# Kernel optimization log

Measured on AMD Instinct MI355X. Metric: run time of the kernel, lower is better.

The kernel has to match this reference:

```python
import jax, jax.numpy as jnp
import numpy as np

N, IN, H, C = 50000, 128, 256, 64
E_G, E_K = 600000, 800000
MLP_H = H // 2  # multiplier=2 (residual=False)
EPS = 1e-5


def _w(k, i, o):
    return (jax.random.normal(k, (i, o), jnp.float32) * np.float32(1.0 / np.sqrt(i)))


def setup_inputs() -> dict:
    key = jax.random.key(0)
    ks = jax.random.split(key, 32)
    inp = {
        "feat": jax.random.normal(ks[0], (N, IN), jnp.float32),
        "g_src": jax.random.randint(ks[1], (E_G,), 0, N, jnp.int32),
        "g_dst": jax.random.randint(ks[2], (E_G,), 0, N, jnp.int32),
        "k_src": jax.random.randint(ks[3], (E_K,), 0, N, jnp.int32),
        "k_dst": jax.random.randint(ks[4], (E_K,), 0, N, jnp.int32),
        # local GraphSAGE: 3 SAGEConv layers (IN->H, H->H, H->H)
        "lw_self_0": _w(ks[5], IN, H), "lw_neigh_0": _w(ks[6], IN, H), "lb_0": jnp.zeros((H,), jnp.float32),
        "lw_self_1": _w(ks[7], H, H),  "lw_neigh_1": _w(ks[8], H, H),  "lb_1": jnp.zeros((H,), jnp.float32),
        "lw_self_2": _w(ks[9], H, H),  "lw_neigh_2": _w(ks[10], H, H), "lb_2": jnp.zeros((H,), jnp.float32),
        # global GraphSAGE: 2 SAGEConv layers (IN->H, H->H)
        "gw_self_0": _w(ks[11], IN, H), "gw_neigh_0": _w(ks[12], IN, H), "gb_0": jnp.zeros((H,), jnp.float32),
        "gw_self_1": _w(ks[13], H, H),  "gw_neigh_1": _w(ks[14], H, H),  "gb_1": jnp.zeros((H,), jnp.float32),
        # MLP head: Linear(2H -> MLP_H), BatchNorm1d(MLP_H), ReLU, Linear(MLP_H -> C)
        "mlp_w1": _w(ks[15], 2 * H, MLP_H), "mlp_b1": jnp.zeros((MLP_H,), jnp.float32),
        "bn_gamma": jnp.ones((MLP_H,), jnp.float32), "bn_beta": jnp.zeros((MLP_H,), jnp.float32),
        "mlp_w2": _w(ks[16], MLP_H, C), "mlp_b2": jnp.zeros((C,), jnp.float32),
    }
    return inp


def sage_conv(src, dst, h, w_self, w_neigh, b):
    # DGL SAGEConv, mean aggregator: fc_self(h) + fc_neigh(mean_{u in N(v)} h_u) + bias
    msg = h[src]                                             # [E, d] irregular gather
    agg = jax.ops.segment_sum(msg, dst, num_segments=N)      # [N, d] irregular scatter-add
    deg = jax.ops.segment_sum(jnp.ones(src.shape, h.dtype), dst, num_segments=N)
    h_neigh = agg / jnp.maximum(deg, 1.0)[:, None]           # isolated nodes -> 0
    return h @ w_self + h_neigh @ w_neigh + b


def batch_norm(x, gamma, beta):
    mu = jnp.mean(x, axis=0)
    var = jnp.mean(jnp.square(x - mu), axis=0)  # biased var, as in torch BN forward
    return gamma * (x - mu) * jax.lax.rsqrt(var + EPS) + beta


def reference(feat, g_src, g_dst, k_src, k_dst,
              lw_self_0, lw_neigh_0, lb_0, lw_self_1, lw_neigh_1, lb_1,
              lw_self_2, lw_neigh_2, lb_2,
              gw_self_0, gw_neigh_0, gb_0, gw_self_1, gw_neigh_1, gb_1,
              mlp_w1, mlp_b1, bn_gamma, bn_beta, mlp_w2, mlp_b2):
    # local GraphSAGE (3 layers, relu between; dropout = identity in eval)
    h = feat
    h = jax.nn.relu(sage_conv(g_src, g_dst, h, lw_self_0, lw_neigh_0, lb_0))
    h = jax.nn.relu(sage_conv(g_src, g_dst, h, lw_self_1, lw_neigh_1, lb_1))
    local_emb = sage_conv(g_src, g_dst, h, lw_self_2, lw_neigh_2, lb_2)
    # global GraphSAGE on knn graph (2 layers)
    h = feat
    h = jax.nn.relu(sage_conv(k_src, k_dst, h, gw_self_0, gw_neigh_0, gb_0))
    global_emb = sage_conv(k_src, k_dst, h, gw_self_1, gw_neigh_1, gb_1)
    # fuse + BatchNorm-MLP head
    x = jnp.concatenate([local_emb, global_emb], axis=1)     # [N, 2H]
    x = x @ mlp_w1 + mlp_b1
    x = jax.nn.relu(batch_norm(x, bn_gamma, bn_beta))
    return x @ mlp_w2 + mlp_b2                               # [N, C]
```

## Files before the change

kernel.cpp:

```cpp
#include <hip/hip_runtime.h>

#define NN   50000
#define IN_F 128
#define HF   256
#define COUT 64
#define MLPH 128
#define EG   600000
#define EK   800000
#define RNG  6250
#define CAPG 80000
#define CAPK 106000
#define BN_EPS 1e-5f

typedef __attribute__((ext_vector_type(8))) short short8;
typedef __attribute__((ext_vector_type(8))) unsigned short ushort8;
typedef __attribute__((ext_vector_type(4))) float f32x4;

__device__ __forceinline__ unsigned short f2bf(float f) {
  union { float f; unsigned int u; } v; v.f = f;
  unsigned int r = v.u + 0x7FFFu + ((v.u >> 16) & 1u);
  return (unsigned short)(r >> 16);
}
__device__ __forceinline__ float bf2f(unsigned short s) {
  union { unsigned int u; float f; } v; v.u = ((unsigned int)s) << 16;
  return v.f;
}

__device__ __forceinline__ void gload_lds16(const void* g, void* l) {
  __builtin_amdgcn_global_load_lds((const __attribute__((address_space(1))) void*)g,
                                   (__attribute__((address_space(3))) void*)l, 16, 0, 0);
}

struct WDesc { const float* src; int rows; int cshift; int kofs; int ldk; int dofs; };
struct WPack { WDesc d[12]; };

__global__ __launch_bounds__(256) void prep_kernel(const float* __restrict__ feat,
                                                   unsigned short* __restrict__ featbf,
                                                   WPack p, unsigned short* __restrict__ wts) {
  int b = blockIdx.x;
  if (b < 3126) {
    int i = b * 256 + threadIdx.x;
    if (i < NN * IN_F / 8) {
      float4 a = *reinterpret_cast<const float4*>(&feat[i * 8]);
      float4 c = *reinterpret_cast<const float4*>(&feat[i * 8 + 4]);
      ushort8 o;
      o[0] = f2bf(a.x); o[1] = f2bf(a.y); o[2] = f2bf(a.z); o[3] = f2bf(a.w);
      o[4] = f2bf(c.x); o[5] = f2bf(c.y); o[6] = f2bf(c.z); o[7] = f2bf(c.w);
      *reinterpret_cast<ushort8*>(&featbf[i * 8]) = o;
    }
  } else {
    int wb = b - 3126;
    WDesc w = p.d[wb >> 5];
    int xb = wb & 31;
    int total = w.rows << w.cshift;
    int cmask = (1 << w.cshift) - 1;
    for (int idx = xb * 256 + threadIdx.x; idx < total; idx += 32 * 256) {
      int r = idx >> w.cshift, c = idx & cmask;
      wts[w.dofs + (size_t)c * w.ldk + w.kofs + r] = f2bf(w.src[idx]);
    }
  }
}

__global__ __launch_bounds__(128) void fuse_w_kernel(
    const float* __restrict__ wl2s, const float* __restrict__ wl2n,
    const float* __restrict__ wg1s, const float* __restrict__ wg1n,
    const float* __restrict__ w1, const float* __restrict__ bl2,
    const float* __restrict__ bg1, const float* __restrict__ b1,
    unsigned short* __restrict__ wf, float* __restrict__ bfused) {
  int b = blockIdx.x;
  int c = threadIdx.x;
  __shared__ float row[256];
  if (b < 1024) {
    int seg = b >> 8, i = b & 255;
    const float* W = (seg == 0) ? wl2s : (seg == 1) ? wl2n : (seg == 2) ? wg1s : wg1n;
    const float* w1b = w1 + ((seg < 2) ? 0 : 256) * MLPH;
    row[c] = W[i * 256 + c];
    row[c + 128] = W[i * 256 + 128 + c];
    __syncthreads();
    float acc = 0.f;
    for (int o = 0; o < 256; ++o) acc += row[o] * w1b[o * MLPH + c];
    wf[(size_t)c * 1024 + seg * 256 + i] = f2bf(acc);
  } else {
    float acc = b1[c];
    for (int o = 0; o < 256; ++o) acc += bl2[o] * w1[o * MLPH + c];
    for (int o = 0; o < 256; ++o) acc += bg1[o] * w1[(256 + o) * MLPH + c];
    bfused[c] = acc;
  }
}

__global__ __launch_bounds__(256) void bucket_kernel(const int* __restrict__ g_src,
                                                     const int* __restrict__ g_dst,
                                                     const int* __restrict__ k_src,
                                                     const int* __restrict__ k_dst,
                                                     int* __restrict__ gcnt,
                                                     unsigned* __restrict__ bkt_g,
                                                     unsigned* __restrict__ bkt_k) {
  __shared__ unsigned buf[2048];
  __shared__ int rcnt[8], rbase[8], roff[8];
  const int gr = blockIdx.y;
  const int* src = gr ? k_src : g_src;
  const int* dst = gr ? k_dst : g_dst;
  unsigned* bkt = gr ? bkt_k : bkt_g;
  const int CAP = gr ? CAPK : CAPG;
  const int E = gr ? EK : EG;
  int* gc = gcnt + gr * 8;
  const int tid = threadIdx.x;
  const int e0 = blockIdx.x * 2048;
  if (e0 >= E) return;
  if (tid < 8) rcnt[tid] = 0;
  __syncthreads();
  unsigned vloc[8];
  int rloc[8], ploc[8];
#pragma unroll
  for (int i = 0; i < 8; ++i) {
    int e = e0 + i * 256 + tid;
    rloc[i] = -1;
    if (e < E) {
      int d = dst[e], s = src[e];
      int r = d / RNG;
      vloc[i] = ((unsigned)d << 16) | (unsigned)s;
      rloc[i] = r;
      ploc[i] = atomicAdd(&rcnt[r], 1);
    }
  }
  __syncthreads();
  if (tid == 0) {
    int acc = 0;
#pragma unroll
    for (int r = 0; r < 8; ++r) { roff[r] = acc; acc += rcnt[r]; }
  }
  __syncthreads();
#pragma unroll
  for (int i = 0; i < 8; ++i)
    if (rloc[i] >= 0) buf[roff[rloc[i]] + ploc[i]] = vloc[i];
  __syncthreads();
  if (tid < 8) rbase[tid] = atomicAdd(&gc[tid], rcnt[tid]);
  __syncthreads();
#pragma unroll
  for (int r = 0; r < 8; ++r) {
    int len = rcnt[r];
    unsigned* dstp = bkt + (size_t)r * CAP + rbase[r];
    for (int i = tid; i < len; i += 256) dstp[i] = buf[roff[r] + i];
  }
}

__global__ __launch_bounds__(256) void count_bucket(const unsigned* __restrict__ bkt_g,
                                                    const unsigned* __restrict__ bkt_k,
                                                    const int* __restrict__ gcnt,
                                                    int* __restrict__ cnt_g,
                                                    int* __restrict__ cnt_k, int CC) {
  __shared__ int hist[RNG];
  const int r = blockIdx.x, gr = blockIdx.y, z = blockIdx.z;
  const unsigned* b = (gr ? bkt_k : bkt_g) + (size_t)r * (gr ? CAPK : CAPG);
  int* cnt = gr ? cnt_k : cnt_g;
  const int n = gcnt[gr * 8 + r];
  const unsigned lo = r * RNG;
  for (int i = threadIdx.x; i < RNG; i += 256) hist[i] = 0;
  __syncthreads();
  for (int i = z * 256 + threadIdx.x; i < n; i += CC * 256) {
    unsigned d = (b[i] >> 16) - lo;
    atomicAdd(&hist[d], 1);
  }
  __syncthreads();
  for (int i = threadIdx.x; i < RNG; i += 256) {
    int v = hist[i];
    if (v) atomicAdd(&cnt[lo + i], v);
  }
}

__global__ __launch_bounds__(256) void scan_partial2(const int* __restrict__ cnt_g,
                                                     const int* __restrict__ cnt_k,
                                                     int* __restrict__ part, int n) {
  const int* cnt = blockIdx.y ? cnt_k : cnt_g;
  int* pp = part + blockIdx.y * 256;
  int i = blockIdx.x * 256 + threadIdx.x;
  int v = (i < n) ? cnt[i] : 0;
  __shared__ int ws[4];
  int lane = threadIdx.x & 63, wid = threadIdx.x >> 6;
  int x = v;
#pragma unroll
  for (int d = 1; d < 64; d <<= 1) { int y = __shfl_up(x, d, 64); if (lane >= d) x += y; }
  if (lane == 63) ws[wid] = x;
  __syncthreads();
  if (threadIdx.x == 0) pp[blockIdx.x] = ws[0] + ws[1] + ws[2] + ws[3];
}

__global__ __launch_bounds__(256) void scan_block2(int* __restrict__ part, int np) {
  int* pp = part + blockIdx.x * 256;
  __shared__ int ws[4];
  int tid = threadIdx.x, lane = tid & 63, wid = tid >> 6;
  int v = (tid < np) ? pp[tid] : 0;
  int x = v;
#pragma unroll
  for (int d = 1; d < 64; d <<= 1) { int y = __shfl_up(x, d, 64); if (lane >= d) x += y; }
  if (lane == 63) ws[wid] = x;
  __syncthreads();
  int add = 0;
#pragma unroll
  for (int k = 0; k < 4; ++k) if (k < wid) add += ws[k];
  if (tid < np) pp[tid] = x - v + add;
}

__global__ __launch_bounds__(256) void scan_final2(const int* __restrict__ cnt_g,
                                                   const int* __restrict__ cnt_k,
                                                   const int* __restrict__ part,
                                                   int* __restrict__ off_g,
                                                   int* __restrict__ off_k,
                                                   float* __restrict__ invg,
                                                   float* __restrict__ invk, int n) {
  const int* cnt = blockIdx.y ? cnt_k : cnt_g;
  const int* pp = part + blockIdx.y * 256;
  int* off = blockIdx.y ? off_k : off_g;
  float* inv = blockIdx.y ? invk : invg;
  int total = blockIdx.y ? EK : EG;
  int i = blockIdx.x * 256 + threadIdx.x;
  int v = (i < n) ? cnt[i] : 0;
  __shared__ int ws[4];
  int lane = threadIdx.x & 63, wid = threadIdx.x >> 6;
  int x = v;
#pragma unroll
  for (int d = 1; d < 64; d <<= 1) { int y = __shfl_up(x, d, 64); if (lane >= d) x += y; }
  if (lane == 63) ws[wid] = x;
  __syncthreads();
  int add = pp[blockIdx.x];
#pragma unroll
  for (int k = 0; k < 4; ++k) if (k < wid) add += ws[k];
  if (i < n) {
    off[i] = x - v + add;
    inv[i] = 1.0f / fmaxf((float)v, 1.0f);
  }
  if (i == 0) off[n] = total;
}

__global__ __launch_bounds__(256) void fill_bucket(const unsigned* __restrict__ bkt_g,
                                                   const unsigned* __restrict__ bkt_k,
                                                   const int* __restrict__ gcnt,
                                                   const int* __restrict__ off_g,
                                                   const int* __restrict__ off_k,
                                                   int* __restrict__ cur_g,
                                                   int* __restrict__ cur_k,
                                                   unsigned short* __restrict__ e16g,
                                                   unsigned short* __restrict__ e16k, int FC) {
  const int r = blockIdx.x, gr = blockIdx.y, z = blockIdx.z;
  const unsigned* b = (gr ? bkt_k : bkt_g) + (size_t)r * (gr ? CAPK : CAPG);
  const int* off = gr ? off_k : off_g;
  int* cur = gr ? cur_k : cur_g;
  unsigned short* e16 = gr ? e16k : e16g;
  const int n = gcnt[gr * 8 + r];
  for (int i = z * 256 + (int)threadIdx.x; i < n; i += FC * 256) {
    unsigned v = b[i];
    int d = v >> 16;
    int pz = atomicAdd(&cur[d], 1);
    e16[off[d] + pz] = (unsigned short)(v & 0xffffu);
  }
}

template <int DLOG2>
__global__ __launch_bounds__(256) void csr_aggregate(const unsigned short* __restrict__ h,
                                                     const int* __restrict__ off,
                                                     const unsigned short* __restrict__ esrc,
                                                     const float* __restrict__ inv,
                                                     unsigned short* __restrict__ out) {
  constexpr int TPN = (1 << DLOG2) / 8;
  constexpr int NPB = 256 / TPN;
  int node = blockIdx.x * NPB + ((int)threadIdx.x / TPN);
  int lane = threadIdx.x & (TPN - 1);
  if (node >= NN) return;
  int s = off[node], e = off[node + 1];
  float acc[8] = {0.f, 0.f, 0.f, 0.f, 0.f, 0.f, 0.f, 0.f};
  int j = s;
  for (; j + 3 < e; j += 4) {
    int s0 = esrc[j], s1 = esrc[j + 1], s2 = esrc[j + 2], s3 = esrc[j + 3];
    ushort8 v0 = *reinterpret_cast<const ushort8*>(&h[((size_t)s0 << DLOG2) + lane * 8]);
    ushort8 v1 = *reinterpret_cast<const ushort8*>(&h[((size_t)s1 << DLOG2) + lane * 8]);
    ushort8 v2 = *reinterpret_cast<const ushort8*>(&h[((size_t)s2 << DLOG2) + lane * 8]);
    ushort8 v3 = *reinterpret_cast<const ushort8*>(&h[((size_t)s3 << DLOG2) + lane * 8]);
#pragma unroll
    for (int i = 0; i < 8; ++i) acc[i] += bf2f(v0[i]);
#pragma unroll
    for (int i = 0; i < 8; ++i) acc[i] += bf2f(v1[i]);
#pragma unroll
    for (int i = 0; i < 8; ++i) acc[i] += bf2f(v2[i]);
#pragma unroll
    for (int i = 0; i < 8; ++i) acc[i] += bf2f(v3[i]);
  }
  for (; j < e; ++j) {
    int s0 = esrc[j];
    ushort8 v0 = *reinterpret_cast<const ushort8*>(&h[((size_t)s0 << DLOG2) + lane * 8]);
#pragma unroll
    for (int i = 0; i < 8; ++i) acc[i] += bf2f(v0[i]);
  }
  float sc = inv[node];
  ushort8 o;
#pragma unroll
  for (int i = 0; i < 8; ++i) o[i] = f2bf(acc[i] * sc);
  *reinterpret_cast<ushort8*>(&out[((size_t)node << DLOG2) + lane * 8]) = o;
}

template <int K1, int K2, bool RELU, bool OUT_BF16>
__global__ __launch_bounds__(256) void gemm_gl(
    const unsigned short* __restrict__ A1, const unsigned short* __restrict__ A2,
    const unsigned short* __restrict__ Bt, const float* __restrict__ bias,
    void* __restrict__ outv, int ldo, int nrows) {
  constexpr int KTOT = K1 + K2;
  constexpr int KT = KTOT / 64;
  __shared__ char smem[32768];
  unsigned short* sA = (unsigned short*)smem;
  unsigned short* sB = sA + 8192;

  const int t = threadIdx.x;
  const int lane = t & 63;
  const int w = t >> 6;
  const int wm = (w & 1) * 64, wn = (w >> 1) * 64;
  const int row0 = blockIdx.y * 128;
  const int n0 = blockIdx.x * 128;

  const int srow = (w << 5) + (lane >> 3);
  const int schunk = (lane & 7) << 3;

  f32x4 acc[4][4] = {};

  for (int kt = 0; kt < KT; ++kt) {
    const int kbase = kt * 64;
    const unsigned short* Asrc = (kbase < K1) ? A1 : A2;
    const int kA = (kbase < K1) ? kbase : (kbase - K1);
    const int lda = (kbase < K1) ? K1 : K2;
#pragma unroll
    for (int q = 0; q < 4; ++q) {
      int rA = srow + q * 8;
      int rowg = row0 + rA;
      if (rowg >= nrows) rowg = nrows - 1;
      gload_lds16(Asrc + (size_t)rowg * lda + kA + schunk,
                  sA + ((w << 5) + q * 8) * 64);
      gload_lds16(Bt + (size_t)(n0 + rA) * KTOT + kbase + schunk,
                  sB + ((w << 5) + q * 8) * 64);
    }
    __syncthreads();
#pragma unroll
    for (int kk = 0; kk < 2; ++kk) {
      const int ko = kk * 32 + (lane >> 4) * 8;
      short8 a[4], b[4];
#pragma unroll
      for (int mi = 0; mi < 4; ++mi)
        a[mi] = *reinterpret_cast<const short8*>(&sA[(wm + mi * 16 + (lane & 15)) * 64 + ko]);
#pragma unroll
      for (int ni = 0; ni < 4; ++ni)
        b[ni] = *reinterpret_cast<const short8*>(&sB[(wn + ni * 16 + (lane & 15)) * 64 + ko]);
#pragma unroll
      for (int mi = 0; mi < 4; ++mi)
#pragma unroll
        for (int ni = 0; ni < 4; ++ni)
          acc[mi][ni] = __builtin_amdgcn_mfma_f32_16x16x32_bf16(a[mi], b[ni], acc[mi][ni], 0, 0, 0);
    }
    __syncthreads();
  }

  float* Co = (float*)smem;
#pragma unroll
  for (int h = 0; h < 2; ++h) {
    __syncthreads();
    if ((w >> 1) == h) {
#pragma unroll
      for (int mi = 0; mi < 4; ++mi)
#pragma unroll
        for (int ni = 0; ni < 4; ++ni) {
          int col = ni * 16 + (lane & 15);
          int rowb = wm + mi * 16 + (lane >> 4) * 4;
#pragma unroll
          for (int j = 0; j < 4; ++j) Co[(rowb + j) * 64 + col] = acc[mi][ni][j];
        }
    }
    __syncthreads();
    int sr = t >> 1, cb = (t & 1) * 32;
    int r = row0 + sr;
    if (r < nrows) {
      float v[32];
#pragma unroll
      for (int i = 0; i < 32; ++i) {
        v[i] = Co[sr * 64 + cb + i] + bias[n0 + h * 64 + cb + i];
        if (RELU) v[i] = fmaxf(v[i], 0.f);
      }
      if (OUT_BF16) {
        unsigned short* dst = (unsigned short*)outv + (size_t)r * ldo + n0 + h * 64 + cb;
#pragma unroll
        for (int q = 0; q < 4; ++q) {
          ushort8 o;
#pragma unroll
          for (int i = 0; i < 8; ++i) o[i] = f2bf(v[q * 8 + i]);
          *reinterpret_cast<ushort8*>(dst + q * 8) = o;
        }
      } else {
        float* dst = (float*)outv + (size_t)r * ldo + n0 + h * 64 + cb;
#pragma unroll
        for (int q = 0; q < 8; ++q) {
          float4 o = make_float4(v[4 * q], v[4 * q + 1], v[4 * q + 2], v[4 * q + 3]);
          *reinterpret_cast<float4*>(dst + 4 * q) = o;
        }
      }
    }
  }
}

__global__ __launch_bounds__(256) void gemm_gl4(
    const unsigned short* __restrict__ A0, const unsigned short* __restrict__ A1,
    const unsigned short* __restrict__ A2, const unsigned short* __restrict__ A3,
    const unsigned short* __restrict__ Bt, const float* __restrict__ bias,
    float* __restrict__ outv, int nrows) {
  constexpr int KTOT = 1024;
  constexpr int KT = 16;
  __shared__ char smem[32768];
  unsigned short* sA = (unsigned short*)smem;
  unsigned short* sB = sA + 8192;

  const int t = threadIdx.x;
  const int lane = t & 63;
  const int w = t >> 6;
  const int wm = (w & 1) * 64, wn = (w >> 1) * 64;
  const int row0 = blockIdx.y * 128;

  const int srow = (w << 5) + (lane >> 3);
  const int schunk = (lane & 7) << 3;

  f32x4 acc[4][4] = {};

  for (int kt = 0; kt < KT; ++kt) {
    const int seg = kt >> 2;
    const unsigned short* Asrc = (seg == 0) ? A0 : (seg == 1) ? A1 : (seg == 2) ? A2 : A3;
    const int kA = (kt & 3) * 64;
#pragma unroll
    for (int q = 0; q < 4; ++q) {
      int rA = srow + q * 8;
      int rowg = row0 + rA;
      if (rowg >= nrows) rowg = nrows - 1;
      gload_lds16(Asrc + (size_t)rowg * 256 + kA + schunk,
                  sA + ((w << 5) + q * 8) * 64);
      gload_lds16(Bt + (size_t)rA * KTOT + kt * 64 + schunk,
                  sB + ((w << 5) + q * 8) * 64);
    }
    __syncthreads();
#pragma unroll
    for (int kk = 0; kk < 2; ++kk) {
      const int ko = kk * 32 + (lane >> 4) * 8;
      short8 a[4], b[4];
#pragma unroll
      for (int mi = 0; mi < 4; ++mi)
        a[mi] = *reinterpret_cast<const short8*>(&sA[(wm + mi * 16 + (lane & 15)) * 64 + ko]);
#pragma unroll
      for (int ni = 0; ni < 4; ++ni)
        b[ni] = *reinterpret_cast<const short8*>(&sB[(wn + ni * 16 + (lane & 15)) * 64 + ko]);
#pragma unroll
      for (int mi = 0; mi < 4; ++mi)
#pragma unroll
        for (int ni = 0; ni < 4; ++ni)
          acc[mi][ni] = __builtin_amdgcn_mfma_f32_16x16x32_bf16(a[mi], b[ni], acc[mi][ni], 0, 0, 0);
    }
    __syncthreads();
  }

  float* Co = (float*)smem;
#pragma unroll
  for (int h = 0; h < 2; ++h) {
    __syncthreads();
    if ((w >> 1) == h) {
#pragma unroll
      for (int mi = 0; mi < 4; ++mi)
#pragma unroll
        for (int ni = 0; ni < 4; ++ni) {
          int col = ni * 16 + (lane & 15);
          int rowb = wm + mi * 16 + (lane >> 4) * 4;
#pragma unroll
          for (int j = 0; j < 4; ++j) Co[(rowb + j) * 64 + col] = acc[mi][ni][j];
        }
    }
    __syncthreads();
    int sr = t >> 1, cb = (t & 1) * 32;
    int r = row0 + sr;
    if (r < nrows) {
      float* dst = outv + (size_t)r * MLPH + h * 64 + cb;
#pragma unroll
      for (int q = 0; q < 8; ++q) {
        float4 o;
        o.x = Co[sr * 64 + cb + 4 * q + 0] + bias[h * 64 + cb + 4 * q + 0];
        o.y = Co[sr * 64 + cb + 4 * q + 1] + bias[h * 64 + cb + 4 * q + 1];
        o.z = Co[sr * 64 + cb + 4 * q + 2] + bias[h * 64 + cb + 4 * q + 2];
        o.w = Co[sr * 64 + cb + 4 * q + 3] + bias[h * 64 + cb + 4 * q + 3];
        *reinterpret_cast<float4*>(dst + 4 * q) = o;
      }
    }
  }
}

__global__ __launch_bounds__(256) void bn_stats_kernel(const float* __restrict__ x,
                                                       float* __restrict__ sums,
                                                       float* __restrict__ sumsq) {
  int c = threadIdx.x & 127;
  int rbase = (blockIdx.x * 256 + threadIdx.x) >> 7;
  int stride = (gridDim.x * 256) >> 7;
  float s = 0.f, s2 = 0.f;
  for (int r = rbase; r < NN; r += stride) {
    float v = x[(size_t)r * 128 + c];
    s += v;
    s2 += v * v;
  }
  __shared__ float ls[256], ls2[256];
  ls[threadIdx.x] = s;
  ls2[threadIdx.x] = s2;
  __syncthreads();
  if (threadIdx.x < 128) {
    s = ls[threadIdx.x] + ls[threadIdx.x + 128];
    s2 = ls2[threadIdx.x] + ls2[threadIdx.x + 128];
    atomicAdd(&sums[c], s);
    atomicAdd(&sumsq[c], s2);
  }
}

__global__ __launch_bounds__(128) void bn_finalize_kernel(float* __restrict__ stats,
                                                          const float* __restrict__ gamma,
                                                          const float* __restrict__ beta) {
  int c = threadIdx.x;
  float mu = stats[c] * (1.0f / NN);
  float var = stats[128 + c] * (1.0f / NN) - mu * mu;
  var = fmaxf(var, 0.f);
  float sc = gamma[c] * rsqrtf(var + BN_EPS);
  stats[256 + c] = sc;
  stats[384 + c] = beta[c] - mu * sc;
}

template <int K1, bool RELU>
__global__ __launch_bounds__(256) void gemm_mfma_bn(
    const float* __restrict__ A1v, const unsigned short* __restrict__ Bt,
    const float* __restrict__ bias, const float* __restrict__ bnscale,
    const float* __restrict__ bnshift, float* __restrict__ outv, int ldo, int nrows) {
  constexpr int KT = K1 / 64;
  constexpr int LDT = 72;
  __shared__ char smem[2 * 64 * LDT * 2];
  unsigned short* As = (unsigned short*)smem;
  unsigned short* Bs = As + 64 * LDT;
  float* Co = (float*)smem;
  constexpr int LDC = 68;

  const int t = threadIdx.x;
  const int lane = t & 63;
  const int w = t >> 6;
  const int wm = (w & 1) * 32, wn = (w >> 1) * 32;
  const int row0 = blockIdx.y * 64;
  const int n0 = blockIdx.x * 64;

  const int sr = t >> 2;
  const int skc = (t & 3) * 16;
  int rg = row0 + sr;
  if (rg >= nrows) rg = nrows - 1;

  f32x4 acc[2][2] = {};

  for (int kt = 0; kt < KT; ++kt) {
    const int kbase = kt * 64;
    {
      const float* xb = A1v + (size_t)rg * K1 + kbase + skc;
      ushort8 o0, o1;
#pragma unroll
      for (int i = 0; i < 8; ++i) {
        float v = xb[i] * bnscale[kbase + skc + i] + bnshift[kbase + skc + i];
        o0[i] = f2bf(fmaxf(v, 0.f));
      }
#pragma unroll
      for (int i = 0; i < 8; ++i) {
        float v = xb[8 + i] * bnscale[kbase + skc + 8 + i] + bnshift[kbase + skc + 8 + i];
        o1[i] = f2bf(fmaxf(v, 0.f));
      }
      *reinterpret_cast<ushort8*>(&As[sr * LDT + skc]) = o0;
      *reinterpret_cast<ushort8*>(&As[sr * LDT + skc + 8]) = o1;
    }
    {
      const unsigned short* bb = Bt + (size_t)(n0 + sr) * K1 + kbase + skc;
      int4 p0 = *reinterpret_cast<const int4*>(bb);
      int4 p1 = *reinterpret_cast<const int4*>(bb + 8);
      *reinterpret_cast<int4*>(&Bs[sr * LDT + skc]) = p0;
      *reinterpret_cast<int4*>(&Bs[sr * LDT + skc + 8]) = p1;
    }
    __syncthreads();
#pragma unroll
    for (int kk = 0; kk < 2; ++kk) {
      const int ko = kk * 32 + (lane >> 4) * 8;
      short8 a0 = *reinterpret_cast<const short8*>(&As[(wm + (lane & 15)) * LDT + ko]);
      short8 a1 = *reinterpret_cast<const short8*>(&As[(wm + 16 + (lane & 15)) * LDT + ko]);
      short8 b0 = *reinterpret_cast<const short8*>(&Bs[(wn + (lane & 15)) * LDT + ko]);
      short8 b1 = *reinterpret_cast<const short8*>(&Bs[(wn + 16 + (lane & 15)) * LDT + ko]);
      acc[0][0] = __builtin_amdgcn_mfma_f32_16x16x32_bf16(a0, b0, acc[0][0], 0, 0, 0);
      acc[0][1] = __builtin_amdgcn_mfma_f32_16x16x32_bf16(a0, b1, acc[0][1], 0, 0, 0);
      acc[1][0] = __builtin_amdgcn_mfma_f32_16x16x32_bf16(a1, b0, acc[1][0], 0, 0, 0);
      acc[1][1] = __builtin_amdgcn_mfma_f32_16x16x32_bf16(a1, b1, acc[1][1], 0, 0, 0);
    }
    __syncthreads();
  }

#pragma unroll
  for (int mi = 0; mi < 2; ++mi)
#pragma unroll
    for (int ni = 0; ni < 2; ++ni) {
      int col = wn + ni * 16 + (lane & 15);
      int rowb = wm + mi * 16 + (lane >> 4) * 4;
#pragma unroll
      for (int j = 0; j < 4; ++j) Co[(rowb + j) * LDC + col] = acc[mi][ni][j];
    }
  __syncthreads();
  {
    int r = row0 + sr;
    if (r < nrows) {
      float v[16];
#pragma unroll
      for (int i = 0; i < 16; ++i) {
        v[i] = Co[sr * LDC + skc + i] + bias[n0 + skc + i];
        if (RELU) v[i] = fmaxf(v[i], 0.f);
      }
      float* dst = outv + (size_t)r * ldo + n0 + skc;
#pragma unroll
      for (int i = 0; i < 4; ++i) {
        float4 o = make_float4(v[4 * i], v[4 * i + 1], v[4 * i + 2], v[4 * i + 3]);
        *reinterpret_cast<float4*>(dst + 4 * i) = o;
      }
    }
  }
}

extern "C" void kernel_launch(void* const* d_in, const int* in_sizes, int n_in,
                              void* d_out, int out_size, void* d_ws, size_t ws_size,
                              hipStream_t stream) {
  const float* feat = (const float*)d_in[0];
  const int* g_src = (const int*)d_in[1];
  const int* g_dst = (const int*)d_in[2];
  const int* k_src = (const int*)d_in[3];
  const int* k_dst = (const int*)d_in[4];
  const float* lb_0 = (const float*)d_in[7];
  const float* lb_1 = (const float*)d_in[10];
  const float* lb_2 = (const float*)d_in[13];
  const float* gb_0 = (const float*)d_in[16];
  const float* gb_1 = (const float*)d_in[19];
  const float* mlp_b1 = (const float*)d_in[21];
  const float* bn_gamma = (const float*)d_in[22];
  const float* bn_beta = (const float*)d_in[23];
  const float* mlp_b2 = (const float*)d_in[25];
  float* out = (float*)d_out;

  float* xf32 = (float*)d_ws;
  int* cnt_g = (int*)(xf32 + (size_t)NN * 128);
  int* cnt_k = cnt_g + NN;
  int* cur_g = cnt_k + NN;
  int* cur_k = cur_g + NN;
  float* stats = (float*)(cur_k + NN);
  int* gcnt = (int*)(stats + 512);
  float* invg = (float*)(gcnt + 16);
  float* invk = invg + NN;
  int* off_g = (int*)(invk + NN);
  int* off_k = off_g + NN + 4;
  int* part = off_k + NN + 4;
  unsigned* bkt_g = (unsigned*)(part + 512);
  unsigned* bkt_k = bkt_g + 8 * CAPG;
  unsigned short* e16g = (unsigned short*)(bkt_k + 8 * CAPK);
  unsigned short* e16k = e16g + EG;
  unsigned short* featbf = e16k + EK;
  unsigned short* wts = featbf + (size_t)NN * IN_F;
  unsigned short* wf = wts + 598016;
  float* bfused = (float*)(wf + 131072);
  unsigned short* bfA = (unsigned short*)(bfused + 128);
  unsigned short* bfB = bfA + (size_t)NN * HF;
  unsigned short* bfAgg = bfB + (size_t)NN * HF;
  unsigned short* bfD = bfAgg + (size_t)NN * HF;

  const int wL0 = 0, wL1 = 65536, wG0 = 327680, wH2 = 589824;

  dim3 blk(256);
  const int NB = (NN + 255) / 256;
  const int MB = (NN + 127) / 128;
  const dim3 gridH(2, MB);
  const dim3 grid4(1, MB);
  const int agg128_blocks = (NN + 15) / 16;
  const int agg256_blocks = (NN + 7) / 8;
  const int BKB = (EK + 2047) / 2048;
  const int CC = 8;
  const int FC = 16;

  hipMemsetAsync(cnt_g, 0, (size_t)(4 * NN) * sizeof(int) + 512 * sizeof(float) + 16 * sizeof(int),
                 stream);

  WPack p;
  p.d[0] = {(const float*)d_in[5], 128, 8, 0, 256, wL0};
  p.d[1] = {(const float*)d_in[6], 128, 8, 128, 256, wL0};
  p.d[2] = {(const float*)d_in[8], 256, 8, 0, 512, wL1};
  p.d[3] = {(const float*)d_in[9], 256, 8, 256, 512, wL1};
  p.d[4] = {(const float*)d_in[11], 256, 8, 0, 512, 196608};
  p.d[5] = {(const float*)d_in[12], 256, 8, 256, 512, 196608};
  p.d[6] = {(const float*)d_in[14], 128, 8, 0, 256, wG0};
  p.d[7] = {(const float*)d_in[15], 128, 8, 128, 256, wG0};
  p.d[8] = {(const float*)d_in[17], 256, 8, 0, 512, 393216};
  p.d[9] = {(const float*)d_in[18], 256, 8, 256, 512, 393216};
  p.d[10] = {(const float*)d_in[20], 512, 7, 0, 512, 524288};
  p.d[11] = {(const float*)d_in[24], 128, 6, 0, 128, wH2};
  prep_kernel<<<3510, blk, 0, stream>>>(feat, featbf, p, wts);

  fuse_w_kernel<<<1025, 128, 0, stream>>>(
      (const float*)d_in[11], (const float*)d_in[12],
      (const float*)d_in[17], (const float*)d_in[18],
      (const float*)d_in[20], lb_2, gb_1, mlp_b1, wf, bfused);

  bucket_kernel<<<dim3(BKB, 2), blk, 0, stream>>>(g_src, g_dst, k_src, k_dst, gcnt, bkt_g, bkt_k);
  count_bucket<<<dim3(8, 2, CC), blk, 0, stream>>>(bkt_g, bkt_k, gcnt, cnt_g, cnt_k, CC);
  scan_partial2<<<dim3(NB, 2), blk, 0, stream>>>(cnt_g, cnt_k, part, NN);
  scan_block2<<<2, blk, 0, stream>>>(part, NB);
  scan_final2<<<dim3(NB, 2), blk, 0, stream>>>(cnt_g, cnt_k, part, off_g, off_k, invg, invk, NN);
  fill_bucket<<<dim3(8, 2, FC), blk, 0, stream>>>(bkt_g, bkt_k, gcnt, off_g, off_k,
                                                  cur_g, cur_k, e16g, e16k, FC);

  csr_aggregate<7><<<agg128_blocks, blk, 0, stream>>>(featbf, off_g, e16g, invg, bfAgg);
  gemm_gl<128, 128, true, true><<<gridH, blk, 0, stream>>>(
      featbf, bfAgg, wts + wL0, lb_0, bfA, HF, NN);
  csr_aggregate<8><<<agg256_blocks, blk, 0, stream>>>(bfA, off_g, e16g, invg, bfAgg);
  gemm_gl<256, 256, true, true><<<gridH, blk, 0, stream>>>(
      bfA, bfAgg, wts + wL1, lb_1, bfB, HF, NN);
  csr_aggregate<8><<<agg256_blocks, blk, 0, stream>>>(bfB, off_g, e16g, invg, bfD);
  csr_aggregate<7><<<agg128_blocks, blk, 0, stream>>>(featbf, off_k, e16k, invk, bfAgg);
  gemm_gl<128, 128, true, true><<<gridH, blk, 0, stream>>>(
      featbf, bfAgg, wts + wG0, gb_0, bfA, HF, NN);
  csr_aggregate<8><<<agg256_blocks, blk, 0, stream>>>(bfA, off_k, e16k, invk, bfAgg);

  gemm_gl4<<<grid4, blk, 0, stream>>>(bfB, bfD, bfA, bfAgg, wf, bfused, xf32, NN);

  bn_stats_kernel<<<256, blk, 0, stream>>>(xf32, stats, stats + 128);
  bn_finalize_kernel<<<1, 128, 0, stream>>>(stats, bn_gamma, bn_beta);

  gemm_mfma_bn<128, false><<<dim3(1, (NN + 63) / 64), blk, 0, stream>>>(
      xf32, wts + wH2, mlp_b2, stats + 256, stats + 384, out, COUT, NN);
}
```

Baseline: 537.9 us.

## Project before aggregating in final SAGE layers to shrink gather width

Uses linearity of mean aggregation to multiply the last local and global layer inputs by the fused neighbor weights (256->128) before the CSR gather, so the two final aggregations run on 128-wide rows instead of 256. The tail GEMM shrinks from K=1024 to K=512 and adds the pre-aggregated projected terms in its epilogue. This costs two extra GEMM launches and extra bf16 buffers, plus an additional bf16 rounding of the projected rows before aggregation.

```diff
diff --git a/kernel.cpp b/kernel.cpp
--- a/kernel.cpp
+++ b/kernel.cpp
@@ -79,7 +79,11 @@
     __syncthreads();
     float acc = 0.f;
     for (int o = 0; o < 256; ++o) acc += row[o] * w1b[o * MLPH + c];
-    wf[(size_t)c * 1024 + seg * 256 + i] = f2bf(acc);
+    unsigned short v = f2bf(acc);
+    if (seg == 0)      wf[(size_t)c * 512 + i] = v;
+    else if (seg == 2) wf[(size_t)c * 512 + 256 + i] = v;
+    else if (seg == 1) wf[65536 + (size_t)c * 256 + i] = v;
+    else               wf[98304 + (size_t)c * 256 + i] = v;
   } else {
     float acc = b1[c];
     for (int o = 0; o < 256; ++o) acc += bl2[o] * w1[o * MLPH + c];
@@ -401,13 +405,13 @@
   }
 }
 
-__global__ __launch_bounds__(256) void gemm_gl4(
+__global__ __launch_bounds__(256) void gemm_tail512(
     const unsigned short* __restrict__ A0, const unsigned short* __restrict__ A1,
-    const unsigned short* __restrict__ A2, const unsigned short* __restrict__ A3,
     const unsigned short* __restrict__ Bt, const float* __restrict__ bias,
+    const unsigned short* __restrict__ aYL, const unsigned short* __restrict__ aYG,
     float* __restrict__ outv, int nrows) {
-  constexpr int KTOT = 1024;
-  constexpr int KT = 16;
+  constexpr int KTOT = 512;
+  constexpr int KT = 8;
   __shared__ char smem[32768];
   unsigned short* sA = (unsigned short*)smem;
   unsigned short* sB = sA + 8192;
@@ -424,8 +428,7 @@
   f32x4 acc[4][4] = {};
 
   for (int kt = 0; kt < KT; ++kt) {
-    const int seg = kt >> 2;
-    const unsigned short* Asrc = (seg == 0) ? A0 : (seg == 1) ? A1 : (seg == 2) ? A2 : A3;
+    const unsigned short* Asrc = (kt < 4) ? A0 : A1;
     const int kA = (kt & 3) * 64;
 #pragma unroll
     for (int q = 0; q < 4; ++q) {
@@ -478,13 +481,16 @@
     if (r < nrows) {
       float* dst = outv + (size_t)r * MLPH + h * 64 + cb;
 #pragma unroll
-      for (int q = 0; q < 8; ++q) {
-        float4 o;
-        o.x = Co[sr * 64 + cb + 4 * q + 0] + bias[h * 64 + cb + 4 * q + 0];
-        o.y = Co[sr * 64 + cb + 4 * q + 1] + bias[h * 64 + cb + 4 * q + 1];
-        o.z = Co[sr * 64 + cb + 4 * q + 2] + bias[h * 64 + cb + 4 * q + 2];
-        o.w = Co[sr * 64 + cb + 4 * q + 3] + bias[h * 64 + cb + 4 * q + 3];
-        *reinterpret_cast<float4*>(dst + 4 * q) = o;
+      for (int q = 0; q < 4; ++q) {
+        ushort8 ya = *reinterpret_cast<const ushort8*>(&aYL[(size_t)r * MLPH + h * 64 + cb + q * 8]);
+        ushort8 yb = *reinterpret_cast<const ushort8*>(&aYG[(size_t)r * MLPH + h * 64 + cb + q * 8]);
+        float v[8];
+#pragma unroll
+        for (int i = 0; i < 8; ++i)
+          v[i] = Co[sr * 64 + cb + q * 8 + i] + bf2f(ya[i]) + bf2f(yb[i]) +
+                 bias[h * 64 + cb + q * 8 + i];
+        *reinterpret_cast<float4*>(dst + q * 8) = make_float4(v[0], v[1], v[2], v[3]);
+        *reinterpret_cast<float4*>(dst + q * 8 + 4) = make_float4(v[4], v[5], v[6], v[7]);
       }
     }
   }
@@ -649,7 +655,8 @@
   int* cur_k = cur_g + NN;
   float* stats = (float*)(cur_k + NN);
   int* gcnt = (int*)(stats + 512);
-  float* invg = (float*)(gcnt + 16);
+  float* zbias = (float*)(gcnt + 16);
+  float* invg = zbias + 128;
   float* invk = invg + NN;
   int* off_g = (int*)(invk + NN);
   int* off_k = off_g + NN + 4;
@@ -665,22 +672,28 @@
   unsigned short* bfA = (unsigned short*)(bfused + 128);
   unsigned short* bfB = bfA + (size_t)NN * HF;
   unsigned short* bfAgg = bfB + (size_t)NN * HF;
-  unsigned short* bfD = bfAgg + (size_t)NN * HF;
+  unsigned short* bfYL = bfAgg + (size_t)NN * HF;
+  unsigned short* bfYG = bfYL + (size_t)NN * MLPH;
+  unsigned short* bfAYL = bfYG + (size_t)NN * MLPH;
+  unsigned short* bfAYG = bfAYL + (size_t)NN * MLPH;
 
   const int wL0 = 0, wL1 = 65536, wG0 = 327680, wH2 = 589824;
+  const int wfYL = 65536, wfYG = 98304;
 
   dim3 blk(256);
   const int NB = (NN + 255) / 256;
   const int MB = (NN + 127) / 128;
   const dim3 gridH(2, MB);
-  const dim3 grid4(1, MB);
+  const dim3 gridM(1, MB);
   const int agg128_blocks = (NN + 15) / 16;
   const int agg256_blocks = (NN + 7) / 8;
   const int BKB = (EK + 2047) / 2048;
   const int CC = 8;
   const int FC = 16;
 
-  hipMemsetAsync(cnt_g, 0, (size_t)(4 * NN) * sizeof(int) + 512 * sizeof(float) + 16 * sizeof(int),
+  hipMemsetAsync(cnt_g, 0,
+                 (size_t)(4 * NN) * sizeof(int) + 512 * sizeof(float) + 16 * sizeof(int) +
+                     128 * sizeof(float),
                  stream);
 
   WPack p;
@@ -717,13 +730,17 @@
   csr_aggregate<8><<<agg256_blocks, blk, 0, stream>>>(bfA, off_g, e16g, invg, bfAgg);
   gemm_gl<256, 256, true, true><<<gridH, blk, 0, stream>>>(
       bfA, bfAgg, wts + wL1, lb_1, bfB, HF, NN);
-  csr_aggregate<8><<<agg256_blocks, blk, 0, stream>>>(bfB, off_g, e16g, invg, bfD);
+  gemm_gl<256, 0, false, true><<<gridM, blk, 0, stream>>>(
+      bfB, nullptr, wf + wfYL, zbias, bfYL, MLPH, NN);
+  csr_aggregate<7><<<agg128_blocks, blk, 0, stream>>>(bfYL, off_g, e16g, invg, bfAYL);
   csr_aggregate<7><<<agg128_blocks, blk, 0, stream>>>(featbf, off_k, e16k, invk, bfAgg);
   gemm_gl<128, 128, true, true><<<gridH, blk, 0, stream>>>(
       featbf, bfAgg, wts + wG0, gb_0, bfA, HF, NN);
-  csr_aggregate<8><<<agg256_blocks, blk, 0, stream>>>(bfA, off_k, e16k, invk, bfAgg);
-
-  gemm_gl4<<<grid4, blk, 0, stream>>>(bfB, bfD, bfA, bfAgg, wf, bfused, xf32, NN);
+  gemm_gl<256, 0, false, true><<<gridM, blk, 0, stream>>>(
+      bfA, nullptr, wf + wfYG, zbias, bfYG, MLPH, NN);
+  csr_aggregate<7><<<agg128_blocks, blk, 0, stream>>>(bfYG, off_k, e16k, invk, bfAYG);
+
+  gemm_tail512<<<gridM, blk, 0, stream>>>(bfB, bfA, wf, bfused, bfAYL, bfAYG, xf32, NN);
 
   bn_stats_kernel<<<256, blk, 0, stream>>>(xf32, stats, stats + 128);
   bn_finalize_kernel<<<1, 128, 0, stream>>>(stats, bn_gamma, bn_beta);
```

Result: faster. 506.8 us (-5.8%).
